# Kernel optimization log

Measured on AMD Instinct MI355X. Metric: run time of the kernel, lower is better.

The kernel has to match this reference:

```python
import jax, jax.numpy as jnp
import numpy as np

N, C, HW, D = 16, 512, 3136, 512


def setup_inputs() -> dict:
    key = jax.random.key(0)
    ks = jax.random.split(key, 7)
    s_in = 1.0 / np.sqrt(C)
    return {
        "batch_flat": jax.random.normal(ks[0], (N, C, HW), dtype=jnp.float32),
        "Wq": jax.random.uniform(ks[1], (D, C), jnp.float32, -s_in, s_in),
        "bq": jax.random.uniform(ks[2], (D,), jnp.float32, -s_in, s_in),
        "Wk": jax.random.uniform(ks[3], (D, C), jnp.float32, -s_in, s_in),
        "bk": jax.random.uniform(ks[4], (D,), jnp.float32, -s_in, s_in),
        "Wv": jax.random.uniform(ks[5], (D, C), jnp.float32, -s_in, s_in),
        "bv": jax.random.uniform(ks[6], (D,), jnp.float32, -s_in, s_in),
    }


def reference(batch_flat, Wq, bq, Wk, bk, Wv, bv):
    # batch_flat: [N, C, HW] -> x: [N, HW, C]
    x = jnp.transpose(batch_flat, (0, 2, 1))
    Q = jnp.einsum("nsc,dc->nsd", x, Wq) + bq  # [N, HW, D]
    K = jnp.einsum("nsc,dc->nsd", x, Wk) + bk
    V = jnp.einsum("nsc,dc->nsd", x, Wv) + bv
    # scores = Q^T @ K over the HW axis -> [N, D, D]; softmax over last dim
    att = jax.nn.softmax(jnp.einsum("nsd,nse->nde", Q, K), axis=-1)
    # att @ V^T -> [N, D, HW]
    return jnp.einsum("nde,nse->nds", att, V)
```

## Files before the change

kernel.cpp:

```cpp
#include <hip/hip_runtime.h>

#define NB   16
#define CD   512
#define HW0  3136
#define HWP  3200
#define DD   512

typedef _Float16 half8 __attribute__((ext_vector_type(8)));
typedef float    floatx4 __attribute__((ext_vector_type(4)));

__device__ __forceinline__ void load_lds16(const _Float16* g, _Float16* l) {
    __builtin_amdgcn_global_load_lds(
        (__attribute__((address_space(1))) void*)g,
        (__attribute__((address_space(3))) void*)l,
        16, 0, 0);
}

__global__ void transpose_cast_kernel(const float* __restrict__ in,
                                      _Float16* __restrict__ out) {
    __shared__ float tile[32][33];
    const int n  = blockIdx.z;
    const int h0 = blockIdx.x * 32;
    const int c0 = blockIdx.y * 32;
    const int tx = threadIdx.x;
    const int ty = threadIdx.y;
    const float* src = in + (long long)n * CD * HW0;
#pragma unroll
    for (int i = ty; i < 32; i += 8) {
        int hw = h0 + tx;
        float v = (hw < HW0) ? src[(long long)(c0 + i) * HW0 + hw] : 0.f;
        tile[i][tx] = v;
    }
    __syncthreads();
    _Float16* dst = out + (long long)n * HWP * CD;
#pragma unroll
    for (int i = ty; i < 32; i += 8) {
        dst[(long long)(h0 + i) * CD + (c0 + tx)] = (_Float16)tile[tx][i];
    }
}

__global__ void convert_w_kernel(const float* __restrict__ wq, const float* __restrict__ wk,
                                 const float* __restrict__ wv, const float* __restrict__ bq,
                                 const float* __restrict__ bk,
                                 _Float16* __restrict__ w2, _Float16* __restrict__ wvh,
                                 float* __restrict__ b2) {
    int i = blockIdx.x * 256 + threadIdx.x;
    if (i < CD * DD) {
        w2[i]          = (_Float16)wq[i];
        w2[CD * DD + i] = (_Float16)wk[i];
        wvh[i]         = (_Float16)wv[i];
    }
    if (i < DD) { b2[i] = bq[i]; b2[DD + i] = bk[i]; }
}

template <int BIAS_MODE, bool OUT_HALF, bool ZERO_PAD>
__global__ __launch_bounds__(256, 2)
void gemm_tn(const _Float16* __restrict__ A, const _Float16* __restrict__ B,
             void* __restrict__ Cout, const float* __restrict__ bias,
             int K, int nValid, int ldc,
             long long strideA, long long strideB, long long strideC) {
    constexpr int BM = 128, BN = 128, BK = 32;
    __shared__ _Float16 As[BM * BK];
    __shared__ _Float16 Bs[BN * BK];

    const int tid  = threadIdx.x;
    const int wave = tid >> 6;
    const int lane = tid & 63;
    const int bz   = blockIdx.z;
    const int m0   = blockIdx.x * BM;
    const int n0   = blockIdx.y * BN;

    const _Float16* Ab = A + (long long)bz * strideA;
    const _Float16* Bb = B + (long long)bz * strideB;

    const int srow = lane >> 2;
    const int scol = (lane & 3) * 8;
    const _Float16* ga0 = Ab + (long long)(m0 + wave * 32 + srow) * K + scol;
    const _Float16* ga1 = ga0 + (long long)16 * K;
    const _Float16* gb0 = Bb + (long long)(n0 + wave * 32 + srow) * K + scol;
    const _Float16* gb1 = gb0 + (long long)16 * K;
    _Float16* lA0 = As + (wave * 32) * BK;
    _Float16* lA1 = As + (wave * 32 + 16) * BK;
    _Float16* lB0 = Bs + (wave * 32) * BK;
    _Float16* lB1 = Bs + (wave * 32 + 16) * BK;

    floatx4 acc[4][4];
#pragma unroll
    for (int i = 0; i < 4; i++)
#pragma unroll
        for (int j = 0; j < 4; j++) acc[i][j] = (floatx4)0.0f;

    const int wm = (wave >> 1) * 64, wn = (wave & 1) * 64;
    const int frow = lane & 15;
    const int fk   = (lane >> 4) * 8;

    for (int k0 = 0; k0 < K; k0 += BK) {
        load_lds16(ga0, lA0); load_lds16(ga1, lA1);
        load_lds16(gb0, lB0); load_lds16(gb1, lB1);
        ga0 += BK; ga1 += BK; gb0 += BK; gb1 += BK;
        __syncthreads();

        half8 af[4], bf[4];
#pragma unroll
        for (int t = 0; t < 4; t++)
            af[t] = *(const half8*)(As + (wm + t * 16 + frow) * BK + fk);
#pragma unroll
        for (int t = 0; t < 4; t++)
            bf[t] = *(const half8*)(Bs + (wn + t * 16 + frow) * BK + fk);
#pragma unroll
        for (int mt = 0; mt < 4; mt++)
#pragma unroll
            for (int nt = 0; nt < 4; nt++)
                acc[mt][nt] = __builtin_amdgcn_mfma_f32_16x16x32_f16(
                    af[mt], bf[nt], acc[mt][nt], 0, 0, 0);
        __syncthreads();
    }

    const int erow = (lane >> 4) * 4;
    const int ecol = lane & 15;
#pragma unroll
    for (int mt = 0; mt < 4; mt++) {
#pragma unroll
        for (int r = 0; r < 4; r++) {
            const int row = m0 + wm + mt * 16 + erow + r;
#pragma unroll
            for (int nt = 0; nt < 4; nt++) {
                const int col = n0 + wn + nt * 16 + ecol;
                float v = acc[mt][nt][r];
                if (BIAS_MODE == 1) v += bias[row];
                if (BIAS_MODE == 2) v += bias[col];
                const bool valid = (col < nValid);
                const long long idx = (long long)bz * strideC + (long long)row * ldc + col;
                if (OUT_HALF) {
                    if (ZERO_PAD) {
                        ((_Float16*)Cout)[idx] = (_Float16)(valid ? v : 0.f);
                    } else if (valid) {
                        ((_Float16*)Cout)[idx] = (_Float16)v;
                    }
                } else {
                    if (ZERO_PAD) {
                        ((float*)Cout)[idx] = valid ? v : 0.f;
                    } else if (valid) {
                        ((float*)Cout)[idx] = v;
                    }
                }
            }
        }
    }
}

__global__ void softmax_kernel(const float* __restrict__ S, _Float16* __restrict__ att) {
    const int row  = blockIdx.x * 4 + (threadIdx.x >> 6);
    const int lane = threadIdx.x & 63;
    const float* src = S + (long long)row * DD;
    float v[8];
#pragma unroll
    for (int i = 0; i < 8; i++) v[i] = src[lane + i * 64];
    float m = v[0];
#pragma unroll
    for (int i = 1; i < 8; i++) m = fmaxf(m, v[i]);
#pragma unroll
    for (int off = 32; off; off >>= 1) m = fmaxf(m, __shfl_xor(m, off, 64));
    float s = 0.f;
#pragma unroll
    for (int i = 0; i < 8; i++) { v[i] = __expf(v[i] - m); s += v[i]; }
#pragma unroll
    for (int off = 32; off; off >>= 1) s += __shfl_xor(s, off, 64);
    const float inv = 1.0f / s;
    _Float16* dst = att + (long long)row * DD;
#pragma unroll
    for (int i = 0; i < 8; i++) dst[lane + i * 64] = (_Float16)(v[i] * inv);
}

extern "C" void kernel_launch(void* const* d_in, const int* in_sizes, int n_in,
                              void* d_out, int out_size, void* d_ws, size_t ws_size,
                              hipStream_t stream) {
    const float* batch = (const float*)d_in[0];
    const float* Wq = (const float*)d_in[1];
    const float* bq = (const float*)d_in[2];
    const float* Wk = (const float*)d_in[3];
    const float* bk = (const float*)d_in[4];
    const float* Wv = (const float*)d_in[5];
    const float* bv = (const float*)d_in[6];

    char* ws = (char*)d_ws;
    const long long XT_B  = (long long)NB * HWP * CD * 2;
    const long long QKT_B = (long long)NB * 2 * DD * HWP * 2;
    const long long VS_B  = (long long)NB * HWP * DD * 2;
    const long long W2_B  = (long long)2 * DD * CD * 2;
    const long long WVH_B = (long long)DD * CD * 2;

    _Float16* Xt  = (_Float16*)(ws);
    _Float16* QKt = (_Float16*)(ws + XT_B);
    _Float16* Vs  = (_Float16*)(ws + XT_B + QKT_B);
    _Float16* W2  = (_Float16*)(ws + XT_B + QKT_B + VS_B);
    _Float16* Wvh = (_Float16*)(ws + XT_B + QKT_B + VS_B + W2_B);
    float*    b2  = (float*)   (ws + XT_B + QKT_B + VS_B + W2_B + WVH_B);
    float*    S   = (float*)(ws);
    _Float16* att = (_Float16*)(ws + (long long)NB * DD * DD * 4);

    convert_w_kernel<<<dim3((CD * DD + 255) / 256), dim3(256), 0, stream>>>(
        Wq, Wk, Wv, bq, bk, W2, Wvh, b2);

    transpose_cast_kernel<<<dim3(HWP / 32, CD / 32, NB), dim3(32, 8), 0, stream>>>(
        batch, Xt);

    gemm_tn<1, true, true><<<dim3(2 * DD / 128, HWP / 128, NB), dim3(256), 0, stream>>>(
        W2, Xt, (void*)QKt, b2, CD, HW0, HWP,
        0LL, (long long)HWP * CD, (long long)2 * DD * HWP);

    gemm_tn<2, true, false><<<dim3(HWP / 128, DD / 128, NB), dim3(256), 0, stream>>>(
        Xt, Wvh, (void*)Vs, bv, CD, DD, DD,
        (long long)HWP * CD, 0LL, (long long)HWP * DD);

    gemm_tn<0, false, false><<<dim3(DD / 128, DD / 128, NB), dim3(256), 0, stream>>>(
        QKt, QKt + (long long)DD * HWP, (void*)S, nullptr, HWP, DD, DD,
        (long long)2 * DD * HWP, (long long)2 * DD * HWP, (long long)DD * DD);

    softmax_kernel<<<dim3(NB * DD / 4), dim3(256), 0, stream>>>(S, att);

    gemm_tn<0, false, false><<<dim3(DD / 128, HWP / 128, NB), dim3(256), 0, stream>>>(
        att, Vs, d_out, nullptr, DD, HW0, HW0,
        (long long)DD * DD, (long long)HWP * DD, (long long)DD * HW0);
}
```

Before: 474.6 us.

## Remap GEMM blocks for XCD-aware locality and widen transpose tiles

After: 475.0 us. No clear change (+0.1%).

```diff
diff --git a/kernel.cpp b/kernel.cpp
--- a/kernel.cpp
+++ b/kernel.cpp
@@ -7,6 +7,7 @@
 #define DD   512
 
 typedef _Float16 half8 __attribute__((ext_vector_type(8)));
+typedef _Float16 half2v __attribute__((ext_vector_type(2)));
 typedef float    floatx4 __attribute__((ext_vector_type(4)));
 
 __device__ __forceinline__ void load_lds16(const _Float16* g, _Float16* l) {
@@ -18,24 +19,23 @@
 
 __global__ void transpose_cast_kernel(const float* __restrict__ in,
                                       _Float16* __restrict__ out) {
-    __shared__ float tile[32][33];
+    __shared__ float tile[128][65];
     const int n  = blockIdx.z;
-    const int h0 = blockIdx.x * 32;
-    const int c0 = blockIdx.y * 32;
+    const int h0 = blockIdx.x * 64;
+    const int c0 = blockIdx.y * 128;
     const int tx = threadIdx.x;
     const int ty = threadIdx.y;
-    const float* src = in + (long long)n * CD * HW0;
-#pragma unroll
-    for (int i = ty; i < 32; i += 8) {
-        int hw = h0 + tx;
-        float v = (hw < HW0) ? src[(long long)(c0 + i) * HW0 + hw] : 0.f;
-        tile[i][tx] = v;
-    }
+    const float* src = in + (long long)n * CD * HW0 + (long long)c0 * HW0 + h0;
+    const bool valid = (h0 + tx) < HW0;
+#pragma unroll
+    for (int i = ty; i < 128; i += 4)
+        tile[i][tx] = valid ? src[(long long)i * HW0 + tx] : 0.f;
     __syncthreads();
-    _Float16* dst = out + (long long)n * HWP * CD;
-#pragma unroll
-    for (int i = ty; i < 32; i += 8) {
-        dst[(long long)(h0 + i) * CD + (c0 + tx)] = (_Float16)tile[tx][i];
+    _Float16* dst = out + (long long)n * HWP * CD + (long long)h0 * CD + c0;
+#pragma unroll
+    for (int i = ty; i < 64; i += 4) {
+        half2v v = { (_Float16)tile[2 * tx][i], (_Float16)tile[2 * tx + 1][i] };
+        *(half2v*)(dst + (long long)i * CD + 2 * tx) = v;
     }
 }
 
@@ -46,14 +46,14 @@
                                  float* __restrict__ b2) {
     int i = blockIdx.x * 256 + threadIdx.x;
     if (i < CD * DD) {
-        w2[i]          = (_Float16)wq[i];
+        w2[i]           = (_Float16)wq[i];
         w2[CD * DD + i] = (_Float16)wk[i];
-        wvh[i]         = (_Float16)wv[i];
+        wvh[i]          = (_Float16)wv[i];
     }
     if (i < DD) { b2[i] = bq[i]; b2[DD + i] = bk[i]; }
 }
 
-template <int BIAS_MODE, bool OUT_HALF, bool ZERO_PAD>
+template <int BIAS_MODE, bool OUT_HALF, bool ZERO_PAD, int GX, int GY, int ORDER>
 __global__ __launch_bounds__(256, 2)
 void gemm_tn(const _Float16* __restrict__ A, const _Float16* __restrict__ B,
              void* __restrict__ Cout, const float* __restrict__ bias,
@@ -66,9 +66,16 @@
     const int tid  = threadIdx.x;
     const int wave = tid >> 6;
     const int lane = tid & 63;
-    const int bz   = blockIdx.z;
-    const int m0   = blockIdx.x * BM;
-    const int n0   = blockIdx.y * BN;
+
+    const int G = gridDim.x;
+    const int b = blockIdx.x;
+    const int w = (b & 7) * (G >> 3) + (b >> 3);
+    int bx, by, bz;
+    if (ORDER == 0) { bx = w % GX; int r = w / GX; by = r % GY; bz = r / GY; }
+    else            { by = w % GY; int r = w / GY; bx = r % GX; bz = r / GX; }
+
+    const int m0 = bx * BM;
+    const int n0 = by * BN;
 
     const _Float16* Ab = A + (long long)bz * strideA;
     const _Float16* Bb = B + (long long)bz * strideB;
@@ -202,24 +209,24 @@
     convert_w_kernel<<<dim3((CD * DD + 255) / 256), dim3(256), 0, stream>>>(
         Wq, Wk, Wv, bq, bk, W2, Wvh, b2);
 
-    transpose_cast_kernel<<<dim3(HWP / 32, CD / 32, NB), dim3(32, 8), 0, stream>>>(
+    transpose_cast_kernel<<<dim3(HWP / 64, CD / 128, NB), dim3(64, 4), 0, stream>>>(
         batch, Xt);
 
-    gemm_tn<1, true, true><<<dim3(2 * DD / 128, HWP / 128, NB), dim3(256), 0, stream>>>(
+    gemm_tn<1, true, true, 8, 25, 0><<<dim3(8 * 25 * NB), dim3(256), 0, stream>>>(
         W2, Xt, (void*)QKt, b2, CD, HW0, HWP,
         0LL, (long long)HWP * CD, (long long)2 * DD * HWP);
 
-    gemm_tn<2, true, false><<<dim3(HWP / 128, DD / 128, NB), dim3(256), 0, stream>>>(
+    gemm_tn<2, true, false, 25, 4, 1><<<dim3(25 * 4 * NB), dim3(256), 0, stream>>>(
         Xt, Wvh, (void*)Vs, bv, CD, DD, DD,
         (long long)HWP * CD, 0LL, (long long)HWP * DD);
 
-    gemm_tn<0, false, false><<<dim3(DD / 128, DD / 128, NB), dim3(256), 0, stream>>>(
+    gemm_tn<0, false, false, 4, 4, 0><<<dim3(4 * 4 * NB), dim3(256), 0, stream>>>(
         QKt, QKt + (long long)DD * HWP, (void*)S, nullptr, HWP, DD, DD,
         (long long)2 * DD * HWP, (long long)2 * DD * HWP, (long long)DD * DD);
 
     softmax_kernel<<<dim3(NB * DD / 4), dim3(256), 0, stream>>>(S, att);
 
-    gemm_tn<0, false, false><<<dim3(DD / 128, HWP / 128, NB), dim3(256), 0, stream>>>(
+    gemm_tn<0, false, false, 4, 25, 0><<<dim3(4 * 25 * NB), dim3(256), 0, stream>>>(
         att, Vs, d_out, nullptr, DD, HW0, HW0,
         (long long)DD * DD, (long long)HWP * DD, (long long)DD * HW0);
 }
```
